# Optimization experiments

Measured on AMD Instinct MI355X. Metric: run time of the kernel, lower is better.

## Reference

```python
import jax, jax.numpy as jnp
import numpy as np

LIMIT = 7.0      # self.m.limit
ACT_ALPHA = 1.702  # self.m.alpha (GLU sigmoid slope)
R = 8
LORA_ALPHA = 16.0
SCALING = LORA_ALPHA / R
E, H, F = 8, 2048, 1024
D = 2 * F
B, S, K = 2, 1024, 4


def setup_inputs() -> dict:
    key = jax.random.key(0)
    ks = jax.random.split(key, 12)
    w = 0.02  # realistic weight scale
    return {
        "hidden_states": jax.random.normal(ks[0], (B, S, H), jnp.float32),
        "routing_weights": jax.random.uniform(ks[1], (B * S, K), jnp.float32),
        "gate_up_proj": jax.random.normal(ks[2], (E, H, D), jnp.float32) * w,
        "gate_up_proj_bias": jax.random.normal(ks[3], (E, D), jnp.float32) * w,
        "down_proj": jax.random.normal(ks[4], (E, F, H), jnp.float32) * w,
        "down_proj_bias": jax.random.normal(ks[5], (E, H), jnp.float32) * w,
        "lora_gate_up_A": jax.random.normal(ks[6], (E, H, R), jnp.float32) * w,
        "lora_gate_up_B": jax.random.normal(ks[7], (E, R, D), jnp.float32) * w,
        "lora_down_A": jax.random.normal(ks[8], (E, F, R), jnp.float32) * w,
        "lora_down_B": jax.random.normal(ks[9], (E, R, H), jnp.float32) * w,
        "router_indices": jax.random.randint(ks[10], (B * S, K), 0, E, jnp.int64),
    }


def reference(hidden_states, routing_weights, gate_up_proj, gate_up_proj_bias,
              down_proj, down_proj_bias, lora_gate_up_A, lora_gate_up_B,
              lora_down_A, lora_down_B, router_indices):
    b, s, h = hidden_states.shape
    x = hidden_states.reshape(-1, h)  # [T,H]
    # Combined per-(expert,token) routing weight: sum over top-k slots that hit expert e.
    onehot = jax.nn.one_hot(router_indices, E, dtype=x.dtype)        # [T,K,E]
    w = jnp.einsum('tke,tk->et', onehot, routing_weights)            # [E,T]
    # gate_up projection with inline LoRA (per expert, all tokens; masked by w later)
    lora1 = jnp.einsum('etr,erd->etd', jnp.einsum('th,ehr->etr', x, lora_gate_up_A), lora_gate_up_B)
    gate_up = jnp.einsum('th,ehd->etd', x, gate_up_proj) + SCALING * lora1 + gate_up_proj_bias[:, None, :]
    gate = jnp.minimum(gate_up[..., ::2], LIMIT)                     # [E,T,F]
    up = jnp.clip(gate_up[..., 1::2], -LIMIT, LIMIT)
    glu = gate * jax.nn.sigmoid(gate * ACT_ALPHA)
    gated = (up + 1.0) * glu                                         # [E,T,F]
    # down projection with inline LoRA
    lora2 = jnp.einsum('etr,erh->eth', jnp.einsum('etf,efr->etr', gated, lora_down_A), lora_down_B)
    out = jnp.einsum('etf,efh->eth', gated, down_proj) + SCALING * lora2 + down_proj_bias[:, None, :]
    # scatter-combine: weight each expert output and sum over experts
    next_states = jnp.einsum('et,eth->th', w, out)                   # [T,H]
    return next_states.reshape(b, s, h)
```

## Files before the change

kernel.cpp:

```cpp
#include <hip/hip_runtime.h>
#include <stdint.h>


typedef short bf16x8 __attribute__((ext_vector_type(8)));
typedef float f32x4 __attribute__((ext_vector_type(4)));

__device__ __forceinline__ short bf16r(float f) {
  uint32_t u = __float_as_uint(f);
  u += 0x7fffu + ((u >> 16) & 1u);
  return (short)(u >> 16);
}

__device__ __forceinline__ float bf16f(short s) {
  uint32_t u = ((uint32_t)(uint16_t)s) << 16;
  return __uint_as_float(u);
}

__device__ __forceinline__ void load_lds16(const void* g, void* l) {
  __builtin_amdgcn_global_load_lds((const __attribute__((address_space(1))) void*)g,
                                   (__attribute__((address_space(3))) void*)l,
                                   16, 0, 0);
}

__global__ void k_route(const int* __restrict__ idx_raw, const float* __restrict__ rw,
                        float* __restrict__ w, int* __restrict__ cnt, int* __restrict__ list,
                        int* __restrict__ tok_nh, int* __restrict__ tok_pair) {
  __shared__ int s_nz;
  const int tid = threadIdx.x;
  if (tid == 0) s_nz = 0;
  __syncthreads();
  int found = 0;
  for (int i = tid; i < 4096; i += 256) found |= idx_raw[2 * i + 1];
  if (found) atomicOr(&s_nz, 1);
  __syncthreads();
  const bool is64 = (s_nz == 0);

  const int t = blockIdx.x * 256 + tid;
  int ek[4]; float rk[4];
#pragma unroll
  for (int k = 0; k < 4; k++) {
    ek[k] = is64 ? idx_raw[2 * (t * 4 + k)] : idx_raw[t * 4 + k];
    rk[k] = rw[t * 4 + k];
  }
  int j = 0;
#pragma unroll
  for (int e = 0; e < 8; e++) {
    float s = 0.f;
#pragma unroll
    for (int k = 0; k < 4; k++) s += (ek[k] == e) ? rk[k] : 0.f;
    w[e * 2048 + t] = s;
    if (s != 0.f) {
      int slot = atomicAdd(&cnt[e], 1);
      list[e * 2048 + slot] = t;
      tok_pair[t * 4 + j] = (e << 16) | slot;
      j++;
    }
  }
  tok_nh[t] = j;
}

__global__ void k_prefix(const int* __restrict__ cnt, int* __restrict__ offs,
                         int* __restrict__ wl) {
  const int tid = threadIdx.x;
  __shared__ int sc[8];
  if (tid < 8) sc[tid] = cnt[tid];
  __syncthreads();
  if (tid == 0) {
    int s = 0;
    for (int e = 0; e < 8; e++) { offs[e] = s; s += sc[e]; }
    offs[8] = s;
  }
  const int j = tid >> 3, e = tid & 7;
  const int nb = (sc[e] + 255) >> 8;
  wl[tid] = (j < nb * 8) ? ((e << 6) | j) : -1;
}

__global__ void k_wprep(const float* __restrict__ W, const float* __restrict__ A,
                        const float* __restrict__ Bm, short* __restrict__ O,
                        int Kd, int Nd) {
  const int e = blockIdx.z;
  const float* We = W + (size_t)e * Kd * Nd;
  const float* Ae = A + (size_t)e * Kd * 8;
  const float* Be = Bm + (size_t)e * 8 * Nd;
  short* Oe = O + (size_t)e * Kd * Nd;
  __shared__ float tile[64][33];
  __shared__ float As[64][9];
  __shared__ float Bs[8][32];
  const int n0 = blockIdx.x * 32, k0 = blockIdx.y * 64;
  {
    const int rr = threadIdx.x >> 3;
    const int cc = (threadIdx.x & 7) * 4;
#pragma unroll
    for (int h = 0; h < 2; h++) {
      float4 v = *(const float4*)(We + (size_t)(k0 + rr + 32 * h) * Nd + n0 + cc);
      tile[rr + 32 * h][cc + 0] = v.x;
      tile[rr + 32 * h][cc + 1] = v.y;
      tile[rr + 32 * h][cc + 2] = v.z;
      tile[rr + 32 * h][cc + 3] = v.w;
    }
  }
  {
    int kk = threadIdx.x >> 3, r = threadIdx.x & 7;
    As[kk][r] = Ae[(size_t)(k0 + kk) * 8 + r];
    As[kk + 32][r] = Ae[(size_t)(k0 + kk + 32) * 8 + r];
  }
  {
    int rr = threadIdx.x >> 5, nn = threadIdx.x & 31;
    Bs[rr][nn] = Be[(size_t)rr * Nd + n0 + nn];
  }
  __syncthreads();
  const int n2 = threadIdx.x >> 3;
  const int kg = (threadIdx.x & 7) * 8;
  float bl[8];
#pragma unroll
  for (int r = 0; r < 8; r++) bl[r] = Bs[r][n2];
  short ov[8];
#pragma unroll
  for (int i = 0; i < 8; i++) {
    const int k = kg + i;
    float v = tile[k][n2];
    float l = 0.f;
#pragma unroll
    for (int r = 0; r < 8; r++) l += As[k][r] * bl[r];
    ov[i] = bf16r(v + 2.0f * l);
  }
  *(bf16x8*)(Oe + (size_t)(n0 + n2) * Kd + k0 + kg) = *(bf16x8*)ov;
}

__global__ void k_xconv(const float* __restrict__ x, short* __restrict__ xb) {
  const int i = (blockIdx.x * 256 + threadIdx.x) * 4;
  float4 v = *(const float4*)(x + i);
  short4 s;
  s.x = bf16r(v.x); s.y = bf16r(v.y); s.z = bf16r(v.z); s.w = bf16r(v.w);
  *(short4*)(xb + i) = s;
}


#define MM_S(AARR, BARR, MG, NG) \
  _Pragma("unroll") \
  for (int s_ = 0; s_ < 2; ++s_) \
    _Pragma("unroll") \
    for (int f_ = 0; f_ < 4; ++f_) \
      _Pragma("unroll") \
      for (int g_ = 0; g_ < 2; ++g_) \
        acc[(MG) + f_][(NG) + g_] = __builtin_amdgcn_mfma_f32_16x16x32_bf16( \
            AARR[f_][s_], BARR[g_][s_], acc[(MG) + f_][(NG) + g_], 0, 0, 0);

template <int KDIM, bool GATHER, bool GLU>
__global__ __launch_bounds__(512) void k_gemmG(
    const short* __restrict__ Abuf, const short* __restrict__ Bbuf,
    const float* __restrict__ bias, const int* __restrict__ cnt,
    const int* __restrict__ offs, const int* __restrict__ wl,
    const int* __restrict__ list, short* __restrict__ outbuf) {
  constexpr int KT = KDIM / 64;

  __shared__ __align__(16) short sA[2 * 256 * 64];
  __shared__ __align__(16) short sB[2 * 256 * 64];
  constexpr int SLOT = 256 * 64;
  constexpr int HALF = 128 * 64;

  const int tid = threadIdx.x;
  const int lane = tid & 63;
  const int wv = tid >> 6;
  const int wr = wv >> 2;
  const int wc = wv & 3;
  const int lm = lane & 15;
  const int quad = lane >> 4;

  const int srow = tid >> 3;
  const int scol = ((tid & 7) ^ (srow & 7)) * 8;

  const int rbA = (wr * 128 + lm) * 64;
  const int rbB = (wc * 64 + lm) * 64;
  const int c0 = ((0 + quad) ^ (lane & 7)) * 8;
  const int c1 = ((4 + quad) ^ (lane & 7)) * 8;

  for (int item = blockIdx.x; item < 512; item += 256) {
    const int wit = wl[item];
    if (wit < 0) continue;
    const int e = wit >> 6;
    const int m0 = ((wit >> 3) & 7) * 256;
    const int n0 = (wit & 7) * 256;
    const int M = cnt[e];
    const int off_e = offs[e];
    const short* Bp = Bbuf + (size_t)e * 2048 * KDIM;

    uint32_t offA[4], offB[4];
#pragma unroll
    for (int j = 0; j < 4; ++j) {
      const int r = m0 + srow + 64 * j;
      const int rc = min(r, M - 1);
      if constexpr (GATHER) {
        offA[j] = (uint32_t)list[e * 2048 + rc] * (uint32_t)KDIM + (uint32_t)scol;
      } else {
        offA[j] = (uint32_t)(off_e + rc) * (uint32_t)KDIM + (uint32_t)scol;
      }
      offB[j] = (uint32_t)(n0 + srow + 64 * j) * (uint32_t)KDIM + (uint32_t)scol;
    }

    auto stageA = [&](int slot, int h, int kt) {
      short* d = sA + slot * SLOT + h * HALF + tid * 8;
      load_lds16(Abuf + offA[2 * h] + kt * 64, d);
      load_lds16(Abuf + offA[2 * h + 1] + kt * 64, d + 4096);
    };
    auto stageB = [&](int slot, int h, int kt) {
      short* d = sB + slot * SLOT + h * HALF + tid * 8;
      load_lds16(Bp + offB[2 * h] + kt * 64, d);
      load_lds16(Bp + offB[2 * h + 1] + kt * 64, d + 4096);
    };

    auto rdA = [&](int slot, int mg, bf16x8 (&a)[4][2]) {
#pragma unroll
      for (int f = 0; f < 4; ++f) {
        const short* p = sA + slot * SLOT + rbA + (mg + f) * 1024;
        a[f][0] = *(const bf16x8*)(p + c0);
        a[f][1] = *(const bf16x8*)(p + c1);
      }
    };
    auto rdB = [&](int slot, int ng, bf16x8 (&b)[2][2]) {
#pragma unroll
      for (int g = 0; g < 2; ++g) {
        const short* p = sB + slot * SLOT + rbB + (ng + g) * 1024;
        b[g][0] = *(const bf16x8*)(p + c0);
        b[g][1] = *(const bf16x8*)(p + c1);
      }
    };

    f32x4 acc[8][4];
#pragma unroll
    for (int i = 0; i < 8; ++i)
#pragma unroll
      for (int j = 0; j < 4; ++j) acc[i][j] = (f32x4){0.f, 0.f, 0.f, 0.f};

    asm volatile("s_waitcnt vmcnt(0)" ::: "memory");

    stageA(0, 0, 0); stageA(0, 1, 0);
    stageB(0, 0, 0); stageB(0, 1, 0);
    {
      const int k1 = (KT > 1) ? 1 : 0;
      stageB(1, 0, k1); stageB(1, 1, k1);
    }
    asm volatile("s_waitcnt vmcnt(4)" ::: "memory");
    asm volatile("s_barrier" ::: "memory");

    bf16x8 aLo[4][2], aHi[4][2], bLo[2][2], bHi[2][2];

#pragma unroll 1
    for (int t = 0; t < KT; ++t) {
      const int slot = t & 1;
      const int tA = min(t + 1, KT - 1);
      const int tB = min(t + 2, KT - 1);
      rdA(slot, 0, aLo);
      rdB(slot, 0, bLo);
      rdB(slot, 2, bHi);
      rdA(slot, 4, aHi);
      stageA(slot ^ 1, 0, tA); stageA(slot ^ 1, 1, tA);
      __builtin_amdgcn_s_setprio(1);
      MM_S(aLo, bLo, 0, 0);
      MM_S(aLo, bHi, 0, 2);
      __builtin_amdgcn_s_setprio(0);
      asm volatile("s_barrier" ::: "memory");
      stageB(slot, 0, tB); stageB(slot, 1, tB);
      __builtin_amdgcn_s_setprio(1);
      MM_S(aHi, bLo, 4, 0);
      MM_S(aHi, bHi, 4, 2);
      __builtin_amdgcn_s_setprio(0);
      asm volatile("s_waitcnt vmcnt(4)" ::: "memory");
      asm volatile("s_barrier" ::: "memory");
    }

    if constexpr (GLU) {
      const float* be = bias + e * 2048;
#pragma unroll
      for (int m = 0; m < 8; ++m) {
        const int rbase = m0 + wr * 128 + m * 16 + quad * 4;
#pragma unroll
        for (int g = 0; g < 4; ++g) {
          const int col = n0 + wc * 64 + g * 16 + lm;
          const float bb = be[col];
#pragma unroll
          for (int r = 0; r < 4; ++r) {
            const int slot = rbase + r;
            float val = acc[m][g][r] + bb;
            float other = __shfl_xor(val, 1);
            if (((lane & 1) == 0) && (slot < M)) {
              float gt = fminf(val, 7.f);
              float u = fminf(fmaxf(other, -7.f), 7.f);
              float glu = gt / (1.f + __expf(-1.702f * gt));
              outbuf[(size_t)(off_e + slot) * 1024 + (col >> 1)] = bf16r((u + 1.f) * glu);
            }
          }
        }
      }
    } else {
#pragma unroll
      for (int m = 0; m < 8; ++m) {
#pragma unroll
        for (int r = 0; r < 4; ++r) {
          const int slot = m0 + wr * 128 + m * 16 + quad * 4 + r;
          if (slot >= M) continue;
          short* prow = outbuf + (size_t)(off_e + slot) * 2048;
#pragma unroll
          for (int g = 0; g < 4; ++g) {
            const int h = n0 + wc * 64 + g * 16 + lm;
            prow[h] = bf16r(acc[m][g][r]);
          }
        }
      }
    }
  }
}

__global__ __launch_bounds__(256) void k_combine(
    const short* __restrict__ pairbuf, const float* __restrict__ bias2,
    const float* __restrict__ wbuf, const int* __restrict__ offs,
    const int* __restrict__ tok_nh, const int* __restrict__ tok_pair,
    float* __restrict__ out) {
  const int t = blockIdx.x;
  const int h0 = threadIdx.x * 8;
  const int nh = tok_nh[t];
  float acc[8];
#pragma unroll
  for (int i = 0; i < 8; i++) acc[i] = 0.f;
  for (int j = 0; j < nh; j++) {
    const int p = tok_pair[t * 4 + j];
    const int e = p >> 16, slot = p & 0xffff;
    const float wt = wbuf[e * 2048 + t];
    const bf16x8 v = *(const bf16x8*)(pairbuf + (size_t)(offs[e] + slot) * 2048 + h0);
    const float4 bA = *(const float4*)(bias2 + e * 2048 + h0);
    const float4 bB = *(const float4*)(bias2 + e * 2048 + h0 + 4);
    acc[0] += wt * (bf16f(v[0]) + bA.x);
    acc[1] += wt * (bf16f(v[1]) + bA.y);
    acc[2] += wt * (bf16f(v[2]) + bA.z);
    acc[3] += wt * (bf16f(v[3]) + bA.w);
    acc[4] += wt * (bf16f(v[4]) + bB.x);
    acc[5] += wt * (bf16f(v[5]) + bB.y);
    acc[6] += wt * (bf16f(v[6]) + bB.z);
    acc[7] += wt * (bf16f(v[7]) + bB.w);
  }
  float4 oA = {acc[0], acc[1], acc[2], acc[3]};
  float4 oB = {acc[4], acc[5], acc[6], acc[7]};
  *(float4*)(out + (size_t)t * 2048 + h0) = oA;
  *(float4*)(out + (size_t)t * 2048 + h0 + 4) = oB;
}

extern "C" void kernel_launch(void* const* d_in, const int* in_sizes, int n_in,
                              void* d_out, int out_size, void* d_ws, size_t ws_size,
                              hipStream_t stream) {
  const float* x   = (const float*)d_in[0];
  const float* rw  = (const float*)d_in[1];
  const float* w1  = (const float*)d_in[2];
  const float* b1  = (const float*)d_in[3];
  const float* w2  = (const float*)d_in[4];
  const float* b2  = (const float*)d_in[5];
  const float* a1  = (const float*)d_in[6];
  const float* lb1 = (const float*)d_in[7];
  const float* a2  = (const float*)d_in[8];
  const float* lb2 = (const float*)d_in[9];
  const int* idx   = (const int*)d_in[10];
  float* out = (float*)d_out;

  char* ws = (char*)d_ws;
  int* cnt     = (int*)(ws);
  int* offs    = (int*)(ws + 64);
  int* tok_nh  = (int*)(ws + 128);
  int* wl      = (int*)(ws + 8320);
  float* wbuf  = (float*)(ws + 16384);
  int* list    = (int*)(ws + 81920);
  int* tok_pair= (int*)(ws + 147456);
  short* Xb    = (short*)(ws + (1ull << 20));
  short* gated = (short*)(ws + 9437184ull);
  short* W2T   = (short*)(ws + 26214400ull);
  short* W1T   = (short*)(ws + 59768832ull);
  short* pairbuf = (short*)(ws + 59768832ull);

  hipMemsetAsync(cnt, 0, 64, stream);

  k_route<<<dim3(8), dim3(256), 0, stream>>>(idx, rw, wbuf, cnt, list, tok_nh, tok_pair);
  k_prefix<<<dim3(1), dim3(512), 0, stream>>>(cnt, offs, wl);
  k_wprep<<<dim3(64, 32, 8), dim3(256), 0, stream>>>(w1, a1, lb1, W1T, 2048, 2048);
  k_wprep<<<dim3(64, 16, 8), dim3(256), 0, stream>>>(w2, a2, lb2, W2T, 1024, 2048);
  k_xconv<<<dim3(4096), dim3(256), 0, stream>>>(x, Xb);
  k_gemmG<2048, true, true><<<dim3(256), dim3(512), 0, stream>>>(
      Xb, W1T, b1, cnt, offs, wl, list, gated);
  k_gemmG<1024, false, false><<<dim3(256), dim3(512), 0, stream>>>(
      gated, W2T, nullptr, cnt, offs, wl, nullptr, pairbuf);
  k_combine<<<dim3(2048), dim3(256), 0, stream>>>(pairbuf, b2, wbuf, offs, tok_nh, tok_pair, out);
}
```

Measured before the change: 416.5 us.

## Triple-buffer B tiles in grouped GEMM and batch routing atomics per block

The grouped GEMM now keeps three LDS slots for B tiles. Each iteration issues all A and B prefetches at its top, which removes the mid-iteration barrier so the MFMA sequence runs uninterrupted. An explicit lgkmcnt wait is added before the end-of-iteration barrier. The routing kernel now counts per-expert slots with shared-memory atomics and does one global atomicAdd per expert per block, cutting global atomic contention. LDS use rises to 160KB per block, which leaves no headroom, and the token order within each expert list changes.

New measurement: 410.9 us. No clear change (-1.3%).

```diff
diff --git a/kernel.cpp b/kernel.cpp
--- a/kernel.cpp
+++ b/kernel.cpp
@@ -26,8 +26,11 @@
                         float* __restrict__ w, int* __restrict__ cnt, int* __restrict__ list,
                         int* __restrict__ tok_nh, int* __restrict__ tok_pair) {
   __shared__ int s_nz;
+  __shared__ int lcnt[8];
+  __shared__ int lbase[8];
   const int tid = threadIdx.x;
   if (tid == 0) s_nz = 0;
+  if (tid < 8) lcnt[tid] = 0;
   __syncthreads();
   int found = 0;
   for (int i = tid; i < 4096; i += 256) found |= idx_raw[2 * i + 1];
@@ -42,6 +45,7 @@
     ek[k] = is64 ? idx_raw[2 * (t * 4 + k)] : idx_raw[t * 4 + k];
     rk[k] = rw[t * 4 + k];
   }
+  int le[4], ls[4];
   int j = 0;
 #pragma unroll
   for (int e = 0; e < 8; e++) {
@@ -50,11 +54,19 @@
     for (int k = 0; k < 4; k++) s += (ek[k] == e) ? rk[k] : 0.f;
     w[e * 2048 + t] = s;
     if (s != 0.f) {
-      int slot = atomicAdd(&cnt[e], 1);
-      list[e * 2048 + slot] = t;
-      tok_pair[t * 4 + j] = (e << 16) | slot;
+      le[j] = e;
+      ls[j] = atomicAdd(&lcnt[e], 1);
       j++;
     }
+  }
+  __syncthreads();
+  if (tid < 8) lbase[tid] = atomicAdd(&cnt[tid], lcnt[tid]);
+  __syncthreads();
+  for (int i = 0; i < j; i++) {
+    const int e = le[i];
+    const int slot = lbase[e] + ls[i];
+    list[e * 2048 + slot] = t;
+    tok_pair[t * 4 + i] = (e << 16) | slot;
   }
   tok_nh[t] = j;
 }
@@ -147,7 +159,7 @@
             AARR[f_][s_], BARR[g_][s_], acc[(MG) + f_][(NG) + g_], 0, 0, 0);
 
 template <int KDIM, bool GATHER, bool GLU>
-__global__ __launch_bounds__(512) void k_gemmG(
+__device__ __forceinline__ void gemm_body(
     const short* __restrict__ Abuf, const short* __restrict__ Bbuf,
     const float* __restrict__ bias, const int* __restrict__ cnt,
     const int* __restrict__ offs, const int* __restrict__ wl,
@@ -155,7 +167,7 @@
   constexpr int KT = KDIM / 64;
 
   __shared__ __align__(16) short sA[2 * 256 * 64];
-  __shared__ __align__(16) short sB[2 * 256 * 64];
+  __shared__ __align__(16) short sB[3 * 256 * 64];
   constexpr int SLOT = 256 * 64;
   constexpr int HALF = 128 * 64;
 
@@ -198,29 +210,33 @@
       offB[j] = (uint32_t)(n0 + srow + 64 * j) * (uint32_t)KDIM + (uint32_t)scol;
     }
 
-    auto stageA = [&](int slot, int h, int kt) {
-      short* d = sA + slot * SLOT + h * HALF + tid * 8;
-      load_lds16(Abuf + offA[2 * h] + kt * 64, d);
-      load_lds16(Abuf + offA[2 * h + 1] + kt * 64, d + 4096);
+    auto stageA2 = [&](short* base, int kt) {
+      short* d = base + tid * 8;
+      load_lds16(Abuf + offA[0] + kt * 64, d);
+      load_lds16(Abuf + offA[1] + kt * 64, d + 4096);
+      load_lds16(Abuf + offA[2] + kt * 64, d + HALF);
+      load_lds16(Abuf + offA[3] + kt * 64, d + HALF + 4096);
     };
-    auto stageB = [&](int slot, int h, int kt) {
-      short* d = sB + slot * SLOT + h * HALF + tid * 8;
-      load_lds16(Bp + offB[2 * h] + kt * 64, d);
-      load_lds16(Bp + offB[2 * h + 1] + kt * 64, d + 4096);
+    auto stageB2 = [&](short* base, int kt) {
+      short* d = base + tid * 8;
+      load_lds16(Bp + offB[0] + kt * 64, d);
+      load_lds16(Bp + offB[1] + kt * 64, d + 4096);
+      load_lds16(Bp + offB[2] + kt * 64, d + HALF);
+      load_lds16(Bp + offB[3] + kt * 64, d + HALF + 4096);
     };
 
-    auto rdA = [&](int slot, int mg, bf16x8 (&a)[4][2]) {
+    auto rdA = [&](const short* base, int mg, bf16x8 (&a)[4][2]) {
 #pragma unroll
       for (int f = 0; f < 4; ++f) {
-        const short* p = sA + slot * SLOT + rbA + (mg + f) * 1024;
+        const short* p = base + rbA + (mg + f) * 1024;
         a[f][0] = *(const bf16x8*)(p + c0);
         a[f][1] = *(const bf16x8*)(p + c1);
       }
     };
-    auto rdB = [&](int slot, int ng, bf16x8 (&b)[2][2]) {
+    auto rdB = [&](const short* base, int ng, bf16x8 (&b)[2][2]) {
 #pragma unroll
       for (int g = 0; g < 2; ++g) {
-        const short* p = sB + slot * SLOT + rbB + (ng + g) * 1024;
+        const short* p = base + rbB + (ng + g) * 1024;
         b[g][0] = *(const bf16x8*)(p + c0);
         b[g][1] = *(const bf16x8*)(p + c1);
       }
@@ -234,39 +250,41 @@
 
     asm volatile("s_waitcnt vmcnt(0)" ::: "memory");
 
-    stageA(0, 0, 0); stageA(0, 1, 0);
-    stageB(0, 0, 0); stageB(0, 1, 0);
-    {
-      const int k1 = (KT > 1) ? 1 : 0;
-      stageB(1, 0, k1); stageB(1, 1, k1);
-    }
+    stageA2(sA, 0);
+    stageB2(sB, 0);
+    stageB2(sB + SLOT, (KT > 1) ? 1 : 0);
     asm volatile("s_waitcnt vmcnt(4)" ::: "memory");
     asm volatile("s_barrier" ::: "memory");
 
     bf16x8 aLo[4][2], aHi[4][2], bLo[2][2], bHi[2][2];
+    int sbr = 0, sbw = 2;
 
 #pragma unroll 1
     for (int t = 0; t < KT; ++t) {
-      const int slot = t & 1;
+      const int s = t & 1;
+      const short* sAr = sA + s * SLOT;
+      short* sAw = sA + (s ^ 1) * SLOT;
+      const short* sBr = sB + sbr * SLOT;
+      short* sBw = sB + sbw * SLOT;
       const int tA = min(t + 1, KT - 1);
       const int tB = min(t + 2, KT - 1);
-      rdA(slot, 0, aLo);
-      rdB(slot, 0, bLo);
-      rdB(slot, 2, bHi);
-      rdA(slot, 4, aHi);
-      stageA(slot ^ 1, 0, tA); stageA(slot ^ 1, 1, tA);
+      rdA(sAr, 0, aLo);
+      rdB(sBr, 0, bLo);
+      rdB(sBr, 2, bHi);
+      rdA(sAr, 4, aHi);
+      stageA2(sAw, tA);
+      stageB2(sBw, tB);
       __builtin_amdgcn_s_setprio(1);
       MM_S(aLo, bLo, 0, 0);
       MM_S(aLo, bHi, 0, 2);
-      __builtin_amdgcn_s_setprio(0);
-      asm volatile("s_barrier" ::: "memory");
-      stageB(slot, 0, tB); stageB(slot, 1, tB);
-      __builtin_amdgcn_s_setprio(1);
       MM_S(aHi, bLo, 4, 0);
       MM_S(aHi, bHi, 4, 2);
       __builtin_amdgcn_s_setprio(0);
       asm volatile("s_waitcnt vmcnt(4)" ::: "memory");
+      asm volatile("s_waitcnt lgkmcnt(0)" ::: "memory");
       asm volatile("s_barrier" ::: "memory");
+      sbr = (sbr == 2) ? 0 : sbr + 1;
+      sbw = (sbw == 2) ? 0 : sbw + 1;
     }
 
     if constexpr (GLU) {
@@ -309,6 +327,21 @@
       }
     }
   }
+}
+
+__global__ __launch_bounds__(512) void k_g1(
+    const short* __restrict__ Abuf, const short* __restrict__ Bbuf,
+    const float* __restrict__ bias, const int* __restrict__ cnt,
+    const int* __restrict__ offs, const int* __restrict__ wl,
+    const int* __restrict__ list, short* __restrict__ outbuf) {
+  gemm_body<2048, true, true>(Abuf, Bbuf, bias, cnt, offs, wl, list, outbuf);
+}
+
+__global__ __launch_bounds__(512) void k_g2(
+    const short* __restrict__ Abuf, const short* __restrict__ Bbuf,
+    const int* __restrict__ cnt, const int* __restrict__ offs,
+    const int* __restrict__ wl, short* __restrict__ outbuf) {
+  gemm_body<1024, false, false>(Abuf, Bbuf, nullptr, cnt, offs, wl, nullptr, outbuf);
 }
 
 __global__ __launch_bounds__(256) void k_combine(
@@ -381,9 +414,7 @@
   k_wprep<<<dim3(64, 32, 8), dim3(256), 0, stream>>>(w1, a1, lb1, W1T, 2048, 2048);
   k_wprep<<<dim3(64, 16, 8), dim3(256), 0, stream>>>(w2, a2, lb2, W2T, 1024, 2048);
   k_xconv<<<dim3(4096), dim3(256), 0, stream>>>(x, Xb);
-  k_gemmG<2048, true, true><<<dim3(256), dim3(512), 0, stream>>>(
-      Xb, W1T, b1, cnt, offs, wl, list, gated);
-  k_gemmG<1024, false, false><<<dim3(256), dim3(512), 0, stream>>>(
-      gated, W2T, nullptr, cnt, offs, wl, nullptr, pairbuf);
+  k_g1<<<dim3(256), dim3(512), 0, stream>>>(Xb, W1T, b1, cnt, offs, wl, list, gated);
+  k_g2<<<dim3(256), dim3(512), 0, stream>>>(gated, W2T, cnt, offs, wl, pairbuf);
   k_combine<<<dim3(2048), dim3(256), 0, stream>>>(pairbuf, b2, wbuf, offs, tok_nh, tok_pair, out);
 }
```
